# Kernel tuning notes

Hardware: AMD Instinct MI355X
Metric: run time of the kernel (lower is better)

## Reference

```python
import jax, jax.numpy as jnp
import numpy as np

B = 512        # batch
TW = 45        # raw wav token length
C = 512        # n_embd
H = 8          # heads
L = 8          # decoder layers
V = 1000       # wav vocab
NLAB = 5       # label vocab
HID = 2048     # 4*C mlp hidden
OH = 768       # output head hidden
WIN, TRAIN = 30, 44
LN_EPS = 1e-5


def _build_mask(t):
    # triangular (strict upper) + sliding-window lower band, tiled 3x3 over segments
    m = np.triu(np.ones((TRAIN, TRAIN), dtype=bool), 1)
    for i in range(WIN, TRAIN):
        m[i, : i - WIN + 1] = True
    m = m[:t, :t]
    return jnp.asarray(np.tile(m, (3, 3)))  # [3t, 3t], True = masked


def setup_inputs() -> dict:
    key = jax.random.key(0)
    ks = iter(jax.random.split(key, 64))

    def rn(shape, s=0.02):
        return jax.random.normal(next(ks), shape, jnp.float32) * s

    inp = {
        'label': jax.random.randint(next(ks), (B, 1), 0, NLAB),
        'wav1': jax.random.randint(next(ks), (B, TW), 0, V),
        'wav2': jax.random.randint(next(ks), (B, TW), 0, V),
        # embeddings
        'emb_label': rn((NLAB, C), 1.0),
        'emb_w1': rn((V, C), 1.0),
        'emb_w2': rn((V, C), 1.0),
        # per-layer stacked params (leading dim L) for lax.scan
        'ln1_g': jnp.ones((L, 3, C), jnp.float32),
        'ln1_b': jnp.zeros((L, 3, C), jnp.float32),
        'ln2_g': jnp.ones((L, 3, C), jnp.float32),
        'ln2_b': jnp.zeros((L, 3, C), jnp.float32),
        'Wq': rn((L, C, C)), 'bq': jnp.zeros((L, C), jnp.float32),
        'Wk': rn((L, C, C)), 'bk': jnp.zeros((L, C), jnp.float32),
        'Wv': rn((L, C, C)), 'bv': jnp.zeros((L, C), jnp.float32),
        'Wp': rn((L, C, C)), 'bp': jnp.zeros((L, C), jnp.float32),
        'W1': rn((L, C, HID)), 'b1': jnp.zeros((L, HID), jnp.float32),
        'W2': rn((L, HID, C)), 'b2': jnp.zeros((L, C), jnp.float32),
        # output heads
        'o1W1': rn((C, OH)), 'o1b1': jnp.zeros((OH,), jnp.float32),
        'o1W2': rn((OH, V)), 'o1b2': jnp.zeros((V,), jnp.float32),
        'o2W1': rn((C, OH)), 'o2b1': jnp.zeros((OH,), jnp.float32),
        'o2W2': rn((OH, V)), 'o2b2': jnp.zeros((V,), jnp.float32),
    }
    return inp


def _forward(label, wav1, wav2, emb_label, emb_w1, emb_w2,
             ln1_g, ln1_b, ln2_g, ln2_b, Wq, bq, Wk, bk, Wv, bv, Wp, bp,
             W1, b1, W2, b2, o1W1, o1b1, o1W2, o1b2, o2W1, o2b1, o2W2, o2b2):
    wav1_src, wav1_tgt = wav1[:, :-1], wav1[:, 1:]
    wav2_src, wav2_tgt = wav2[:, :-1], wav2[:, 1:]
    b, t = wav1_src.shape
    label_rep = jnp.broadcast_to(label, (b, t))

    feat = jnp.concatenate([emb_label[label_rep], emb_w1[wav1_src], emb_w2[wav2_src]], axis=1)  # [B,3t,C]
    mask = _build_mask(t)  # [3t,3t] bool
    hd = C // H

    def ln3(x, g, be):
        # three separate LayerNorms over the 3 equal segments
        xr = x.reshape(b, 3, t, C)
        mu = xr.mean(-1, keepdims=True)
        var = xr.var(-1, keepdims=True)
        xn = (xr - mu) * jax.lax.rsqrt(var + LN_EPS)
        return (xn * g[None, :, None, :] + be[None, :, None, :]).reshape(b, 3 * t, C)

    def layer(x, p):
        g1, be1, g2, be2, wq, bq_, wk, bk_, wv, bv_, wp, bp_, w1, b1_, w2, b2_ = p
        h = ln3(x, g1, be1)
        q = (h @ wq + bq_).reshape(b, 3 * t, H, hd).transpose(0, 2, 1, 3)
        k = (h @ wk + bk_).reshape(b, 3 * t, H, hd).transpose(0, 2, 1, 3)
        v = (h @ wv + bv_).reshape(b, 3 * t, H, hd).transpose(0, 2, 1, 3)
        att = jnp.einsum('bhqd,bhkd->bhqk', q, k) * (1.0 / np.sqrt(hd))
        att = jnp.where(mask[None, None], -jnp.inf, att)
        att = jax.nn.softmax(att, axis=-1)
        y = jnp.einsum('bhqk,bhkd->bhqd', att, v).transpose(0, 2, 1, 3).reshape(b, 3 * t, C)
        x = x + (y @ wp + bp_)
        h2 = ln3(x, g2, be2)
        m = jax.nn.gelu(h2 @ w1 + b1_, approximate=False) @ w2 + b2_
        return x + m, None

    params = (ln1_g, ln1_b, ln2_g, ln2_b, Wq, bq, Wk, bk, Wv, bv, Wp, bp, W1, b1, W2, b2)
    x, _ = jax.lax.scan(layer, feat, params)

    wav1_pred = (x[:, t:2 * t] @ o1W1 + o1b1) @ o1W2 + o1b2  # [B,t,V]
    wav2_pred = (x[:, 2 * t:] @ o2W1 + o2b1) @ o2W2 + o2b2

    def ce(logits, tgt):
        lp = jax.nn.log_softmax(logits.reshape(-1, V).astype(jnp.float32), axis=-1)
        return -jnp.mean(jnp.take_along_axis(lp, tgt.reshape(-1, 1), axis=1))

    return ce(wav1_pred, wav1_tgt) + ce(wav2_pred, wav2_tgt)


def reference(label, wav1, wav2, emb_label, emb_w1, emb_w2,
              ln1_g, ln1_b, ln2_g, ln2_b, Wq, bq, Wk, bk, Wv, bv, Wp, bp,
              W1, b1, W2, b2, o1W1, o1b1, o1W2, o1b2, o2W1, o2b1, o2W2, o2b2):
    return _forward(label, wav1, wav2, emb_label, emb_w1, emb_w2,
                    ln1_g, ln1_b, ln2_g, ln2_b, Wq, bq, Wk, bk, Wv, bv, Wp, bp,
                    W1, b1, W2, b2, o1W1, o1b1, o1W2, o1b2, o2W1, o2b1, o2W2, o2b2)
```

## Files before the change

kernel.cpp:

```cpp
#include <hip/hip_runtime.h>

typedef __attribute__((ext_vector_type(4))) float f32x4;
typedef __attribute__((ext_vector_type(8))) __bf16 bf16x8;
typedef __attribute__((ext_vector_type(4))) __bf16 bf16x4;
typedef __attribute__((ext_vector_type(8))) unsigned short u16x8;

#define NB 512
#define TT 44
#define S3 132
#define CC 512
#define NH 8
#define NL 8
#define NV 1000
#define VP 1024
#define HID 2048
#define OH 768
#define WINW 30
#define QKVN 1536

#define HROWS (NB*TT)

#define WT_OFF   0ull
#define WC1T_OFF 50331648ull
#define WC2T_OFF 51380224ull
#define BC1_OFF  52428800ull
#define BC2_OFF  52432896ull
#define BQKV_OFF 52436992ull
#define LOSS_OFF 52486144ull
#define FIXED_SZ 52666368ull
#define PER_CHB  811008ull

#define LAYER_WELEMS 3145728ull

__device__ inline bf16x8 zero8() { u16x8 z = (u16x8)0; return *(bf16x8*)&z; }

#define STAGE(bufi, ktile) do { \
  _Pragma("unroll") \
  for (int i_ = 0; i_ < 2; ++i_) { \
    int off_ = wid * 2048 + i_ * 1024; \
    int myoff_ = off_ + lane * 16; \
    int row_ = myoff_ >> 6; \
    int colb_ = (myoff_ & 63) ^ ((row_ & 3) << 4); \
    const char* sa_ = (const char*)(A + (arow + row_) * (size_t)K + ((ktile) << 5)) + colb_; \
    const char* sb_ = (const char*)(Bt + (brow + row_) * (size_t)K + ((ktile) << 5)) + colb_; \
    __builtin_amdgcn_global_load_lds((const __attribute__((address_space(1))) void*)sa_, \
        (__attribute__((address_space(3))) void*)((char*)&As[bufi][0] + off_), 16, 0, 0); \
    __builtin_amdgcn_global_load_lds((const __attribute__((address_space(1))) void*)sb_, \
        (__attribute__((address_space(3))) void*)((char*)&Bs[bufi][0] + off_), 16, 0, 0); \
  } \
} while (0)

template<int EPI, typename OutT, typename ResT>
__global__ __launch_bounds__(256) void gemm_bt(
    const __bf16* __restrict__ A, const __bf16* __restrict__ Bt,
    const float* __restrict__ bias, const ResT* __restrict__ resid,
    OutT* __restrict__ C, int M, int N, int K)
{
    __shared__ __bf16 As[3][128 * 32];
    __shared__ __bf16 Bs[3][128 * 32];
    const int tid = threadIdx.x, lane = tid & 63, wid = tid >> 6;
    const int l15 = lane & 15, lk = lane >> 4;
    const int wr = wid >> 1, wc = wid & 1;
    const int swz = l15 & 3;

    const int nwg = gridDim.x * gridDim.y;
    const int orig = blockIdx.y * gridDim.x + blockIdx.x;
    const int qq = nwg >> 3, rr = nwg & 7;
    const int xcd = orig & 7, loc = orig >> 3;
    const int wg = (xcd < rr ? xcd * (qq + 1) : rr * (qq + 1) + (xcd - rr) * qq) + loc;
    const int bn = wg % gridDim.x, bm = wg / gridDim.x;

    f32x4 acc[4][4];
#pragma unroll
    for (int i = 0; i < 4; ++i)
#pragma unroll
        for (int j = 0; j < 4; ++j) acc[i][j] = (f32x4)0.f;

    const size_t arow = (size_t)bm * 128;
    const size_t brow = (size_t)bn * 128;
    const int KT = K >> 5;

    STAGE(0, 0);
    STAGE(1, 1);
    asm volatile("s_waitcnt vmcnt(4)\n\ts_barrier" ::: "memory");

    int cur = 0, stg = 2;
    for (int kt = 0; kt < KT; ++kt) {
        bf16x8 af[4], bfv[4];
#pragma unroll
        for (int mi = 0; mi < 4; ++mi)
            af[mi] = *(const bf16x8*)&As[cur][(wr * 64 + mi * 16 + l15) * 32 + ((lk ^ swz) * 8)];
#pragma unroll
        for (int ni = 0; ni < 4; ++ni)
            bfv[ni] = *(const bf16x8*)&Bs[cur][(wc * 64 + ni * 16 + l15) * 32 + ((lk ^ swz) * 8)];
        bool more = (kt + 2 < KT);
        if (more) STAGE(stg, kt + 2);
#pragma unroll
        for (int mi = 0; mi < 4; ++mi)
#pragma unroll
            for (int ni = 0; ni < 4; ++ni)
                acc[mi][ni] = __builtin_amdgcn_mfma_f32_16x16x32_bf16(af[mi], bfv[ni], acc[mi][ni], 0, 0, 0);
        if (more) { asm volatile("s_waitcnt vmcnt(4)\n\ts_barrier" ::: "memory"); }
        else      { asm volatile("s_waitcnt vmcnt(0)\n\ts_barrier" ::: "memory"); }
        cur = (cur == 2) ? 0 : cur + 1;
        stg = (stg == 2) ? 0 : stg + 1;
    }

#pragma unroll
    for (int mi = 0; mi < 4; ++mi) {
#pragma unroll
        for (int ni = 0; ni < 4; ++ni) {
            int n = bn * 128 + wc * 64 + ni * 16 + l15;
            float bv = (EPI & 1) ? bias[n] : 0.f;
#pragma unroll
            for (int r = 0; r < 4; ++r) {
                int m = bm * 128 + wr * 64 + mi * 16 + lk * 4 + r;
                float v = acc[mi][ni][r] + bv;
                if (EPI & 2) v += (float)resid[(size_t)m * N + n];
                if (EPI & 4) {
                    float u = 0.7978845608f * (v + 0.044715f * v * v * v);
                    float e = __expf(-2.f * fabsf(u));
                    float th = (1.f - e) / (1.f + e);
                    th = (u < 0.f) ? -th : th;
                    v = 0.5f * v * (1.f + th);
                }
                C[(size_t)m * N + n] = (OutT)v;
            }
        }
    }
}

#define KLS 72
#define VTS 168
__global__ __launch_bounds__(256) void attn_k(const __bf16* __restrict__ QKV,
                                              __bf16* __restrict__ Y)
{
    __shared__ __bf16 Kl[144 * KLS];
    __shared__ __bf16 Vt[64 * VTS];
    __shared__ __bf16 Pl[4][16 * VTS];
    const int tid = threadIdx.x, lane = tid & 63, wid = tid >> 6;
    const int l15 = lane & 15, lk = lane >> 4;
    const int bh = blockIdx.x;
    const int b = bh >> 3, h = bh & 7;
    const size_t base = ((size_t)b * S3) * QKVN + h * 64;
    const size_t ybase = ((size_t)b * S3) * CC + h * 64;

    for (int i = tid; i < 144 * 8; i += 256) {
        int s = i >> 3, c = (i & 7) * 8;
        bf16x8 kv = zero8();
        if (s < S3) kv = *(const bf16x8*)(QKV + base + (size_t)s * QKVN + 512 + c);
        *(bf16x8*)&Kl[s * KLS + c] = kv;
    }
    for (int i = tid; i < S3 * 8; i += 256) {
        int s = i >> 3, d0 = (i & 7) * 8;
        bf16x8 vv = *(const bf16x8*)(QKV + base + (size_t)s * QKVN + 1024 + d0);
#pragma unroll
        for (int j = 0; j < 8; ++j) Vt[(d0 + j) * VTS + s] = vv[j];
    }
    for (int i = tid; i < 64 * 36; i += 256) {
        int d = i / 36, s = 132 + (i % 36);
        Vt[d * VTS + s] = (__bf16)0.f;
    }
    for (int i = lane; i < 16 * 24; i += 64) {
        int r = i / 24, c2 = 144 + (i % 24);
        Pl[wid][r * VTS + c2] = (__bf16)0.f;
    }
    __syncthreads();

    for (int qb = wid; qb < 9; qb += 4) {
        int sq = qb * 16 + l15;
        int sqe = sq < S3 ? sq : (S3 - 1);
        bf16x8 qf0 = *(const bf16x8*)(QKV + base + (size_t)sqe * QKVN + 0 * 32 + lk * 8);
        bf16x8 qf1 = *(const bf16x8*)(QKV + base + (size_t)sqe * QKVN + 1 * 32 + lk * 8);
        f32x4 st[9];
#pragma unroll
        for (int kt = 0; kt < 9; ++kt) {
            f32x4 a = (f32x4)0.f;
            bf16x8 kf0 = *(const bf16x8*)&Kl[(kt * 16 + l15) * KLS + 0 * 32 + lk * 8];
            bf16x8 kf1 = *(const bf16x8*)&Kl[(kt * 16 + l15) * KLS + 1 * 32 + lk * 8];
            a = __builtin_amdgcn_mfma_f32_16x16x32_bf16(kf0, qf0, a, 0, 0, 0);
            a = __builtin_amdgcn_mfma_f32_16x16x32_bf16(kf1, qf1, a, 0, 0, 0);
            st[kt] = a;
        }
        int qm = sqe % TT;
        float mx = -1e30f;
#pragma unroll
        for (int kt = 0; kt < 9; ++kt)
#pragma unroll
            for (int r = 0; r < 4; ++r) {
                int sk = kt * 16 + lk * 4 + r;
                float sv = st[kt][r] * 0.125f;
                int kk = sk % TT;
                bool msk = (sk >= S3) || (kk > qm) || (qm >= WINW && kk <= qm - WINW);
                sv = msk ? -INFINITY : sv;
                st[kt][r] = sv;
                mx = fmaxf(mx, sv);
            }
        mx = fmaxf(mx, __shfl_xor(mx, 16));
        mx = fmaxf(mx, __shfl_xor(mx, 32));
        float sum = 0.f;
#pragma unroll
        for (int kt = 0; kt < 9; ++kt)
#pragma unroll
            for (int r = 0; r < 4; ++r) {
                float p = expf(st[kt][r] - mx);
                st[kt][r] = p;
                sum += p;
            }
        sum += __shfl_xor(sum, 16);
        sum += __shfl_xor(sum, 32);
        float inv = 1.f / sum;
#pragma unroll
        for (int kt = 0; kt < 9; ++kt) {
            bf16x4 pk;
#pragma unroll
            for (int r = 0; r < 4; ++r) pk[r] = (__bf16)(st[kt][r] * inv);
            *(bf16x4*)&Pl[wid][l15 * VTS + kt * 16 + lk * 4] = pk;
        }
#pragma unroll
        for (int dt = 0; dt < 4; ++dt) {
            f32x4 o = (f32x4)0.f;
#pragma unroll
            for (int ks = 0; ks < 5; ++ks) {
                bf16x8 pa = *(const bf16x8*)&Pl[wid][l15 * VTS + ks * 32 + lk * 8];
                bf16x8 vb = *(const bf16x8*)&Vt[(dt * 16 + l15) * VTS + ks * 32 + lk * 8];
                o = __builtin_amdgcn_mfma_f32_16x16x32_bf16(pa, vb, o, 0, 0, 0);
            }
            int d = dt * 16 + l15;
#pragma unroll
            for (int r = 0; r < 4; ++r) {
                int sqr = qb * 16 + lk * 4 + r;
                if (sqr < S3) Y[ybase + (size_t)sqr * CC + d] = (__bf16)o[r];
            }
        }
    }
}

__global__ __launch_bounds__(256) void ln3_k(const __bf16* __restrict__ X,
                                             const float* __restrict__ g,
                                             const float* __restrict__ be,
                                             __bf16* __restrict__ Hb)
{
    int row = blockIdx.x * 4 + (threadIdx.x >> 6);
    int lane = threadIdx.x & 63;
    int seg = (row % S3) / TT;
    bf16x8 xv = *(const bf16x8*)(X + (size_t)row * CC + lane * 8);
    float vv[8];
    float s = 0.f, ss = 0.f;
#pragma unroll
    for (int j = 0; j < 8; ++j) { vv[j] = (float)xv[j]; s += vv[j]; ss += vv[j] * vv[j]; }
#pragma unroll
    for (int o = 32; o; o >>= 1) { s += __shfl_xor(s, o); ss += __shfl_xor(ss, o); }
    float mu = s * (1.f / CC);
    float var = ss * (1.f / CC) - mu * mu;
    float rs = rsqrtf(var + 1e-5f);
    const float* gp = g + seg * CC + lane * 8;
    const float* bp = be + seg * CC + lane * 8;
    __bf16* op = Hb + (size_t)row * CC + lane * 8;
#pragma unroll
    for (int j = 0; j < 8; ++j) op[j] = (__bf16)((vv[j] - mu) * rs * gp[j] + bp[j]);
}

__global__ __launch_bounds__(128) void embed_k(const int* __restrict__ label,
                                               const int* __restrict__ wav1,
                                               const int* __restrict__ wav2,
                                               const float* __restrict__ el,
                                               const float* __restrict__ e1,
                                               const float* __restrict__ e2,
                                               __bf16* __restrict__ X, int b0)
{
    int row = blockIdx.x;
    int b = b0 + row / S3, p = row % S3;
    int seg = p / TT, pos = p % TT;
    int idx; const float* src;
    if (seg == 0) { idx = label[b]; src = el; }
    else if (seg == 1) { idx = wav1[b * 45 + pos]; src = e1; }
    else { idx = wav2[b * 45 + pos]; src = e2; }
    float4 v = *((const float4*)(src + (size_t)idx * CC) + threadIdx.x);
    __bf16* dst = X + (size_t)row * CC + threadIdx.x * 4;
    dst[0] = (__bf16)v.x; dst[1] = (__bf16)v.y; dst[2] = (__bf16)v.z; dst[3] = (__bf16)v.w;
}

__global__ void transpose_cast(const float* __restrict__ in, __bf16* __restrict__ out,
                               int R, int Cin, int Np, long long inStride, long long outStride)
{
    __shared__ float t[32][33];
    in += (size_t)blockIdx.z * inStride;
    out += (size_t)blockIdx.z * outStride;
    int r0 = blockIdx.x * 32, c0 = blockIdx.y * 32;
    int tx = threadIdx.x, ty = threadIdx.y;
#pragma unroll
    for (int k2 = 0; k2 < 4; ++k2) {
        int r = r0 + ty + k2 * 8, c = c0 + tx;
        t[ty + k2 * 8][tx] = (r < R && c < Cin) ? in[(size_t)r * Cin + c] : 0.f;
    }
    __syncthreads();
#pragma unroll
    for (int k2 = 0; k2 < 4; ++k2) {
        int c = c0 + ty + k2 * 8, r = r0 + tx;
        if (c < Np && r < R) out[(size_t)c * R + r] = (__bf16)t[tx][ty + k2 * 8];
    }
}

__global__ void cast_k(const float* __restrict__ in, __bf16* __restrict__ out, int n)
{
    int i = blockIdx.x * 256 + threadIdx.x;
    if (i < n) out[i] = (__bf16)in[i];
}

__global__ void build_bqkv(const float* __restrict__ bq, const float* __restrict__ bk,
                           const float* __restrict__ bv, float* __restrict__ out)
{
    int i = blockIdx.x * 256 + threadIdx.x;
    if (i >= NL * QKVN) return;
    int l = i / QKVN, c = i % QKVN;
    float v = (c < 512) ? bq[l * 512 + c] : (c < 1024 ? bk[l * 512 + c - 512] : bv[l * 512 + c - 1024]);
    out[i] = v;
}

__global__ __launch_bounds__(128) void gather_cast(const __bf16* __restrict__ X,
                                                   __bf16* __restrict__ out, int segoff)
{
    int row = blockIdx.x;
    int b = row / TT, s2 = row % TT;
    const uint2* src = (const uint2*)(X + ((size_t)b * S3 + segoff + s2) * CC) + threadIdx.x;
    uint2* dst = (uint2*)(out + (size_t)row * CC) + threadIdx.x;
    *dst = *src;
}

__global__ void combo_bias(const float* __restrict__ b1, const float* __restrict__ W2,
                           const float* __restrict__ b2, float* __restrict__ out)
{
    int v = blockIdx.x * 256 + threadIdx.x;
    if (v >= VP) return;
    float s = 0.f;
    if (v < NV) {
        s = b2[v];
        for (int o = 0; o < OH; ++o) s += b1[o] * W2[o * NV + v];
    }
    out[v] = s;
}

__global__ __launch_bounds__(256) void ce_k(const float* __restrict__ logits,
                                            const int* __restrict__ wav,
                                            float* __restrict__ loss)
{
    int row = blockIdx.x * 4 + (threadIdx.x >> 6);
    int lane = threadIdx.x & 63;
    const float* lg = logits + (size_t)row * VP;
    int b = row / TT, s2 = row % TT;
    int tgt = wav[b * 45 + s2 + 1];
    float m = -1e30f;
    for (int i = lane; i < NV; i += 64) m = fmaxf(m, lg[i]);
#pragma unroll
    for (int o = 32; o; o >>= 1) m = fmaxf(m, __shfl_xor(m, o));
    float sum = 0.f;
    for (int i = lane; i < NV; i += 64) sum += expf(lg[i] - m);
#pragma unroll
    for (int o = 32; o; o >>= 1) sum += __shfl_xor(sum, o);
    if (lane == 0) loss[row] = m + logf(sum) - lg[tgt];
}

__global__ __launch_bounds__(256) void ce_sum(const float* __restrict__ loss, float* __restrict__ out)
{
    float s = 0.f;
    for (int i = threadIdx.x; i < 2 * HROWS; i += 256) s += loss[i];
#pragma unroll
    for (int o = 32; o; o >>= 1) s += __shfl_xor(s, o);
    __shared__ float w4[4];
    if ((threadIdx.x & 63) == 0) w4[threadIdx.x >> 6] = s;
    __syncthreads();
    if (threadIdx.x == 0) out[0] = (w4[0] + w4[1] + w4[2] + w4[3]) * (1.f / HROWS);
}

extern "C" void kernel_launch(void* const* d_in, const int* in_sizes, int n_in,
                              void* d_out, int out_size, void* d_ws, size_t ws_size,
                              hipStream_t stream)
{
    int chb;
    if      (ws_size >= FIXED_SZ + 512ull * PER_CHB) chb = 512;
    else if (ws_size >= FIXED_SZ + 256ull * PER_CHB) chb = 256;
    else if (ws_size >= FIXED_SZ + 128ull * PER_CHB) chb = 128;
    else return;
    const int nch = NB / chb;
    const int crows = chb * S3;
    const int chr = chb * TT;

    const int*   label = (const int*)d_in[0];
    const int*   wav1  = (const int*)d_in[1];
    const int*   wav2  = (const int*)d_in[2];
    const float* el    = (const float*)d_in[3];
    const float* e1    = (const float*)d_in[4];
    const float* e2    = (const float*)d_in[5];
    const float* ln1g  = (const float*)d_in[6];
    const float* ln1b  = (const float*)d_in[7];
    const float* ln2g  = (const float*)d_in[8];
    const float* ln2b  = (const float*)d_in[9];
    const float* Wq    = (const float*)d_in[10];
    const float* bq    = (const float*)d_in[11];
    const float* Wk    = (const float*)d_in[12];
    const float* bk    = (const float*)d_in[13];
    const float* Wv    = (const float*)d_in[14];
    const float* bv    = (const float*)d_in[15];
    const float* Wp    = (const float*)d_in[16];
    const float* bp    = (const float*)d_in[17];
    const float* W1    = (const float*)d_in[18];
    const float* b1    = (const float*)d_in[19];
    const float* W2    = (const float*)d_in[20];
    const float* b2    = (const float*)d_in[21];
    const float* o1W1  = (const float*)d_in[22];
    const float* o1b1  = (const float*)d_in[23];
    const float* o1W2  = (const float*)d_in[24];
    const float* o1b2  = (const float*)d_in[25];
    const float* o2W1  = (const float*)d_in[26];
    const float* o2b1  = (const float*)d_in[27];
    const float* o2W2  = (const float*)d_in[28];
    const float* o2b2  = (const float*)d_in[29];

    char* ws = (char*)d_ws;
    __bf16* WT    = (__bf16*)(ws + WT_OFF);
    __bf16* Wc1T  = (__bf16*)(ws + WC1T_OFF);
    __bf16* Wc2T  = (__bf16*)(ws + WC2T_OFF);
    float*  bc1   = (float*)(ws + BC1_OFF);
    float*  bc2   = (float*)(ws + BC2_OFF);
    float*  bqkv  = (float*)(ws + BQKV_OFF);
    float*  lossb = (float*)(ws + LOSS_OFF);
    __bf16* X     = (__bf16*)(ws + FIXED_SZ);
    __bf16* Hb    = (__bf16*)(ws + FIXED_SZ + (size_t)chb * 135168ull);
    char*   AR    = ws + FIXED_SZ + (size_t)chb * 270336ull;
    __bf16* o1W2T = (__bf16*)(AR + 0);
    __bf16* o2W2T = (__bf16*)(AR + 1572864);
    __bf16* o1W1b = (__bf16*)(AR + 3145728);
    __bf16* o2W1b = (__bf16*)(AR + 3932160);
    __bf16* qkvb   = (__bf16*)AR;
    __bf16* yb_    = Hb;
    __bf16* hidden = (__bf16*)AR;
    float*  logits = (float*)AR;
    __bf16* Xseg   = Hb;
    float*  outF   = (float*)d_out;

    dim3 tb(32, 8);
    transpose_cast<<<dim3(16, 16, NL), tb, 0, stream>>>(Wq, WT + 0,       CC, CC, CC, (long long)CC * CC, (long long)LAYER_WELEMS);
    transpose_cast<<<dim3(16, 16, NL), tb, 0, stream>>>(Wk, WT + 262144,  CC, CC, CC, (long long)CC * CC, (long long)LAYER_WELEMS);
    transpose_cast<<<dim3(16, 16, NL), tb, 0, stream>>>(Wv, WT + 524288,  CC, CC, CC, (long long)CC * CC, (long long)LAYER_WELEMS);
    transpose_cast<<<dim3(16, 16, NL), tb, 0, stream>>>(Wp, WT + 786432,  CC, CC, CC, (long long)CC * CC, (long long)LAYER_WELEMS);
    transpose_cast<<<dim3(16, 64, NL), tb, 0, stream>>>(W1, WT + 1048576, CC, HID, HID, (long long)CC * HID, (long long)LAYER_WELEMS);
    transpose_cast<<<dim3(64, 16, NL), tb, 0, stream>>>(W2, WT + 2097152, HID, CC, CC, (long long)HID * CC, (long long)LAYER_WELEMS);
    transpose_cast<<<dim3(24, 32, 1), tb, 0, stream>>>(o1W2, o1W2T, OH, NV, VP, 0, 0);
    transpose_cast<<<dim3(24, 32, 1), tb, 0, stream>>>(o2W2, o2W2T, OH, NV, VP, 0, 0);
    cast_k<<<(CC * OH + 255) / 256, 256, 0, stream>>>(o1W1, o1W1b, CC * OH);
    cast_k<<<(CC * OH + 255) / 256, 256, 0, stream>>>(o2W1, o2W1b, CC * OH);
    gemm_bt<0, __bf16, float><<<dim3(4, 8), 256, 0, stream>>>(o1W2T, o1W1b, nullptr, nullptr, Wc1T, VP, CC, OH);
    gemm_bt<0, __bf16, float><<<dim3(4, 8), 256, 0, stream>>>(o2W2T, o2W1b, nullptr, nullptr, Wc2T, VP, CC, OH);
    combo_bias<<<VP / 256, 256, 0, stream>>>(o1b1, o1W2, o1b2, bc1);
    combo_bias<<<VP / 256, 256, 0, stream>>>(o2b1, o2W2, o2b2, bc2);
    build_bqkv<<<(NL * QKVN + 255) / 256, 256, 0, stream>>>(bq, bk, bv, bqkv);

    for (int c = 0; c < nch; ++c) {
        int b0 = c * chb;
        embed_k<<<crows, 128, 0, stream>>>(label, wav1, wav2, el, e1, e2, X, b0);

        for (int l = 0; l < NL; ++l) {
            const __bf16* WqkvT = WT + (size_t)l * LAYER_WELEMS;
            const __bf16* WpT   = WT + (size_t)l * LAYER_WELEMS + 786432;
            const __bf16* W1T   = WT + (size_t)l * LAYER_WELEMS + 1048576;
            const __bf16* W2T   = WT + (size_t)l * LAYER_WELEMS + 2097152;

            ln3_k<<<crows / 4, 256, 0, stream>>>(X, ln1g + l * 3 * CC, ln1b + l * 3 * CC, Hb);
            gemm_bt<1, __bf16, float><<<dim3(QKVN / 128, crows / 128), 256, 0, stream>>>(Hb, WqkvT, bqkv + l * QKVN, nullptr, qkvb, crows, QKVN, CC);
            attn_k<<<chb * NH, 256, 0, stream>>>(qkvb, yb_);
            gemm_bt<3, __bf16, __bf16><<<dim3(4, crows / 128), 256, 0, stream>>>(yb_, WpT, bp + l * CC, X, X, crows, CC, CC);
            ln3_k<<<crows / 4, 256, 0, stream>>>(X, ln2g + l * 3 * CC, ln2b + l * 3 * CC, Hb);
            gemm_bt<5, __bf16, float><<<dim3(16, crows / 128), 256, 0, stream>>>(Hb, W1T, b1 + l * HID, nullptr, hidden, crows, HID, CC);
            gemm_bt<3, __bf16, __bf16><<<dim3(4, crows / 128), 256, 0, stream>>>(hidden, W2T, b2 + l * CC, X, X, crows, CC, HID);
        }

        gather_cast<<<chr, 128, 0, stream>>>(X, Xseg, TT);
        gemm_bt<1, float, float><<<dim3(VP / 128, chr / 128), 256, 0, stream>>>(Xseg, Wc1T, bc1, nullptr, logits, chr, VP, CC);
        ce_k<<<chr / 4, 256, 0, stream>>>(logits, wav1 + b0 * 45, lossb + c * chr);
        gather_cast<<<chr, 128, 0, stream>>>(X, Xseg, 2 * TT);
        gemm_bt<1, float, float><<<dim3(VP / 128, chr / 128), 256, 0, stream>>>(Xseg, Wc2T, bc2, nullptr, logits, chr, VP, CC);
        ce_k<<<chr / 4, 256, 0, stream>>>(logits, wav2 + b0 * 45, lossb + HROWS + c * chr);
    }

    ce_sum<<<1, 256, 0, stream>>>(lossb, outF);
}
```

Baseline: 8.053 ms.

## Stage Q in LDS, pair V transpose writes, parallelize combo bias, exact GELU

The attention kernel now stages Q into shared memory alongside K, reducing the padding strides and writing the transposed V two elements at a time. The combo_bias precompute is parallelized across a block per output column with a wave and shared-memory reduction instead of one serial loop per thread. The GELU epilogue switches from a tanh approximation to the exact erf form, matching the reference's approximate=False. Together these target attention load and LDS store costs and setup-kernel latency, at the cost of more LDS per block and a possibly slower erf call.

```diff
diff --git a/kernel.cpp b/kernel.cpp
--- a/kernel.cpp
+++ b/kernel.cpp
@@ -3,6 +3,7 @@
 typedef __attribute__((ext_vector_type(4))) float f32x4;
 typedef __attribute__((ext_vector_type(8))) __bf16 bf16x8;
 typedef __attribute__((ext_vector_type(4))) __bf16 bf16x4;
+typedef __attribute__((ext_vector_type(2))) __bf16 bf16x2;
 typedef __attribute__((ext_vector_type(8))) unsigned short u16x8;
 
 #define NB 512
@@ -117,25 +118,20 @@
                 int m = bm * 128 + wr * 64 + mi * 16 + lk * 4 + r;
                 float v = acc[mi][ni][r] + bv;
                 if (EPI & 2) v += (float)resid[(size_t)m * N + n];
-                if (EPI & 4) {
-                    float u = 0.7978845608f * (v + 0.044715f * v * v * v);
-                    float e = __expf(-2.f * fabsf(u));
-                    float th = (1.f - e) / (1.f + e);
-                    th = (u < 0.f) ? -th : th;
-                    v = 0.5f * v * (1.f + th);
-                }
+                if (EPI & 4) v = 0.5f * v * (1.f + erff(v * 0.70710678118f));
                 C[(size_t)m * N + n] = (OutT)v;
             }
         }
     }
 }
 
-#define KLS 72
-#define VTS 168
+#define KLS 68
+#define VTS 164
 __global__ __launch_bounds__(256) void attn_k(const __bf16* __restrict__ QKV,
                                               __bf16* __restrict__ Y)
 {
     __shared__ __bf16 Kl[144 * KLS];
+    __shared__ __bf16 Ql[144 * KLS];
     __shared__ __bf16 Vt[64 * VTS];
     __shared__ __bf16 Pl[4][16 * VTS];
     const int tid = threadIdx.x, lane = tid & 63, wid = tid >> 6;
@@ -145,24 +141,30 @@
     const size_t base = ((size_t)b * S3) * QKVN + h * 64;
     const size_t ybase = ((size_t)b * S3) * CC + h * 64;
 
-    for (int i = tid; i < 144 * 8; i += 256) {
+    for (int i = tid; i < S3 * 8; i += 256) {
         int s = i >> 3, c = (i & 7) * 8;
-        bf16x8 kv = zero8();
-        if (s < S3) kv = *(const bf16x8*)(QKV + base + (size_t)s * QKVN + 512 + c);
+        bf16x8 qv = *(const bf16x8*)(QKV + base + (size_t)s * QKVN + c);
+        bf16x8 kv = *(const bf16x8*)(QKV + base + (size_t)s * QKVN + 512 + c);
+        *(bf16x8*)&Ql[s * KLS + c] = qv;
         *(bf16x8*)&Kl[s * KLS + c] = kv;
     }
-    for (int i = tid; i < S3 * 8; i += 256) {
-        int s = i >> 3, d0 = (i & 7) * 8;
-        bf16x8 vv = *(const bf16x8*)(QKV + base + (size_t)s * QKVN + 1024 + d0);
-#pragma unroll
-        for (int j = 0; j < 8; ++j) Vt[(d0 + j) * VTS + s] = vv[j];
-    }
-    for (int i = tid; i < 64 * 36; i += 256) {
-        int d = i / 36, s = 132 + (i % 36);
+    for (int i = tid; i < (S3 / 2) * 8; i += 256) {
+        int s2 = i >> 3, d0 = (i & 7) * 8;
+        int s = s2 * 2;
+        bf16x8 v0 = *(const bf16x8*)(QKV + base + (size_t)s * QKVN + 1024 + d0);
+        bf16x8 v1 = *(const bf16x8*)(QKV + base + (size_t)(s + 1) * QKVN + 1024 + d0);
+#pragma unroll
+        for (int j = 0; j < 8; ++j) {
+            bf16x2 pr; pr[0] = v0[j]; pr[1] = v1[j];
+            *(bf16x2*)&Vt[(d0 + j) * VTS + s] = pr;
+        }
+    }
+    for (int i = tid; i < 64 * 32; i += 256) {
+        int d = i >> 5, s = 132 + (i & 31);
         Vt[d * VTS + s] = (__bf16)0.f;
     }
-    for (int i = lane; i < 16 * 24; i += 64) {
-        int r = i / 24, c2 = 144 + (i % 24);
+    for (int i = lane; i < 16 * 20; i += 64) {
+        int r = i / 20, c2 = 144 + (i % 20);
         Pl[wid][r * VTS + c2] = (__bf16)0.f;
     }
     __syncthreads();
@@ -170,8 +172,8 @@
     for (int qb = wid; qb < 9; qb += 4) {
         int sq = qb * 16 + l15;
         int sqe = sq < S3 ? sq : (S3 - 1);
-        bf16x8 qf0 = *(const bf16x8*)(QKV + base + (size_t)sqe * QKVN + 0 * 32 + lk * 8);
-        bf16x8 qf1 = *(const bf16x8*)(QKV + base + (size_t)sqe * QKVN + 1 * 32 + lk * 8);
+        bf16x8 qf0 = *(const bf16x8*)&Ql[(qb * 16 + l15) * KLS + 0 * 32 + lk * 8];
+        bf16x8 qf1 = *(const bf16x8*)&Ql[(qb * 16 + l15) * KLS + 1 * 32 + lk * 8];
         f32x4 st[9];
 #pragma unroll
         for (int kt = 0; kt < 9; ++kt) {
@@ -328,17 +330,23 @@
     *dst = *src;
 }
 
-__global__ void combo_bias(const float* __restrict__ b1, const float* __restrict__ W2,
-                           const float* __restrict__ b2, float* __restrict__ out)
-{
-    int v = blockIdx.x * 256 + threadIdx.x;
+__global__ __launch_bounds__(256) void combo_bias(const float* __restrict__ b1,
+                                                  const float* __restrict__ W2,
+                                                  const float* __restrict__ b2,
+                                                  float* __restrict__ out)
+{
+    int v = blockIdx.x;
     if (v >= VP) return;
     float s = 0.f;
     if (v < NV) {
-        s = b2[v];
-        for (int o = 0; o < OH; ++o) s += b1[o] * W2[o * NV + v];
-    }
-    out[v] = s;
+        for (int o = threadIdx.x; o < OH; o += 256) s += b1[o] * W2[o * NV + v];
+    }
+#pragma unroll
+    for (int o = 32; o; o >>= 1) s += __shfl_xor(s, o);
+    __shared__ float w4[4];
+    if ((threadIdx.x & 63) == 0) w4[threadIdx.x >> 6] = s;
+    __syncthreads();
+    if (threadIdx.x == 0) out[v] = (v < NV ? b2[v] : 0.f) + w4[0] + w4[1] + w4[2] + w4[3];
 }
 
 __global__ __launch_bounds__(256) void ce_k(const float* __restrict__ logits,
@@ -452,8 +460,8 @@
     cast_k<<<(CC * OH + 255) / 256, 256, 0, stream>>>(o2W1, o2W1b, CC * OH);
     gemm_bt<0, __bf16, float><<<dim3(4, 8), 256, 0, stream>>>(o1W2T, o1W1b, nullptr, nullptr, Wc1T, VP, CC, OH);
     gemm_bt<0, __bf16, float><<<dim3(4, 8), 256, 0, stream>>>(o2W2T, o2W1b, nullptr, nullptr, Wc2T, VP, CC, OH);
-    combo_bias<<<VP / 256, 256, 0, stream>>>(o1b1, o1W2, o1b2, bc1);
-    combo_bias<<<VP / 256, 256, 0, stream>>>(o2b1, o2W2, o2b2, bc2);
+    combo_bias<<<VP, 256, 0, stream>>>(o1b1, o1W2, o1b2, bc1);
+    combo_bias<<<VP, 256, 0, stream>>>(o2b1, o2W2, o2b2, bc2);
     build_bqkv<<<(NL * QKVN + 255) / 256, 256, 0, stream>>>(bq, bk, bv, bqkv);
 
     for (int c = 0; c < nch; ++c) {
```

Result: faster. 7.486 ms (-7.0%).
